# Kernel tuning notes

Measured on AMD Instinct MI355X. Metric: run time of the kernel, lower is better.

Reference implementation:

```python
import jax, jax.numpy as jnp
import numpy as np

B = 4096
D = 1024
N = 9000000
TEMPERATURE = 0.1
GAMMA = 0.8
ALPHA = 0.5
EPS = 1e-14


def setup_inputs() -> dict:
    key = jax.random.key(0)
    k1, k2, k3, k4, k5 = jax.random.split(key, 5)
    zis = jax.random.normal(k1, (B, D), dtype=jnp.float32)
    zjs = jax.random.normal(k2, (B, D), dtype=jnp.float32)
    s_I = jax.random.uniform(k3, (N,), dtype=jnp.float32)
    s_T = jax.random.uniform(k4, (N,), dtype=jnp.float32)
    b_I = jnp.zeros((N,), dtype=jnp.float32)
    b_T = jnp.zeros((N,), dtype=jnp.float32)
    ids = jax.random.randint(k5, (B,), 0, N, dtype=jnp.int64 if jax.config.jax_enable_x64 else jnp.int32)
    return {"zis": zis, "zjs": zjs, "s_I": s_I, "s_T": s_T, "b_I": b_I, "b_T": b_T, "ids": ids}


def reference(zis, zjs, s_I, s_T, b_I, b_T, ids):
    sg = jax.lax.stop_gradient
    # L2 normalize embeddings (norm=True path)
    zis = zis / jnp.linalg.norm(zis, axis=1, keepdims=True)
    zjs = zjs / jnp.linalg.norm(zjs, axis=1, keepdims=True)
    sim = jnp.einsum('id,jd->ij', zis, zjs)            # [B, B]
    diag = jnp.diagonal(sim)                            # [B]
    image_diffs = sim - diag[:, None]
    text_diffs = sim - diag[None, :]
    # detached, temperature-scaled diffs (torch .clone().detach_())
    idd = sg(image_diffs) / TEMPERATURE
    tdd = sg(text_diffs) / TEMPERATURE
    # online max tracking (per-id running max b)
    old_b_I = b_I[ids]                                  # gather [B]
    new_b_I = jnp.maximum(idd.max(axis=1), old_b_I)
    old_b_T = b_T[ids]
    new_b_T = jnp.maximum(tdd.max(axis=0), old_b_T)
    mask_neg = 1.0 - jnp.eye(B, dtype=sim.dtype)
    exp_image_diffs = jnp.exp(idd - new_b_I[:, None]) * mask_neg
    exp_text_diffs = jnp.exp(tdd - new_b_T[None, :]) * mask_neg
    g_I = exp_image_diffs.sum(axis=1) / (B - 1)         # [B]
    g_T = exp_text_diffs.sum(axis=0) / (B - 1)          # [B]
    # EMA of softmax denominator with rescaling for new max
    s_I_new = (1.0 - GAMMA) * s_I[ids] * jnp.exp(old_b_I - new_b_I) + GAMMA * g_I
    s_T_new = (1.0 - GAMMA) * s_T[ids] * jnp.exp(old_b_T - new_b_T) + GAMMA * g_T
    # state writes (side effects in torch; computed for fidelity)
    b_I = b_I.at[ids].set(new_b_I)
    b_T = b_T.at[ids].set(new_b_T)
    s_I = s_I.at[ids].set(s_I_new)
    s_T = s_T.at[ids].set(s_T_new)
    s_I_c = jnp.maximum(s_I_new, EPS)
    s_T_c = jnp.maximum(s_T_new, EPS)
    weights_image = exp_image_diffs / s_I_c[:, None]    # detached weights
    weights_text = exp_text_diffs / s_T_c[None, :]
    image_loss = (weights_image * image_diffs).sum(axis=1) / (B - 1)
    text_loss = (weights_text * text_diffs).sum(axis=0) / (B - 1)
    total_loss = ALPHA * image_loss.mean() + (1.0 - ALPHA) * text_loss.mean()
    return total_loss
```

## Files before the change

### kernel.cpp

```cpp
#include <hip/hip_runtime.h>
#include <stdint.h>

#define B_ 4096
#define D_ 1024
#define BM 256
#define BN 128
#define BK 32
#define NT 32
#define TINV 10.0f
#define LOG2E 1.4426950408889634f
#define KE (TINV * LOG2E)
#define INV_BM1 (1.0f / 4095.0f)

typedef __bf16 bf16x8 __attribute__((ext_vector_type(8)));
typedef float f32x4 __attribute__((ext_vector_type(4)));

__device__ __forceinline__ unsigned short f2bf(float x) {
  uint32_t b = __float_as_uint(x);
  b += 0x7FFF + ((b >> 16) & 1);
  return (unsigned short)(b >> 16);
}
__device__ __forceinline__ float bf2f(unsigned short u) {
  return __uint_as_float(((uint32_t)u) << 16);
}

__device__ __forceinline__ void gload16(const void* g, void* l) {
  __builtin_amdgcn_global_load_lds(
      (const __attribute__((address_space(1))) uint32_t*)g,
      (__attribute__((address_space(3))) uint32_t*)l, 16, 0, 0);
}

__global__ __launch_bounds__(256) void k_normalize(const float* __restrict__ zis,
                                                   const float* __restrict__ zjs,
                                                   unsigned short* __restrict__ Abf,
                                                   unsigned short* __restrict__ Bbf) {
  int r = blockIdx.x;
  const float* src;
  unsigned short* dst;
  if (r < B_) { src = zis + (size_t)r * D_; dst = Abf + (size_t)r * D_; }
  else        { src = zjs + (size_t)(r - B_) * D_; dst = Bbf + (size_t)(r - B_) * D_; }
  int t = threadIdx.x;
  float4 v = reinterpret_cast<const float4*>(src)[t];
  float ss = v.x*v.x + v.y*v.y + v.z*v.z + v.w*v.w;
  #pragma unroll
  for (int o = 32; o >= 1; o >>= 1) ss += __shfl_down(ss, o);
  __shared__ float red[4];
  if ((t & 63) == 0) red[t >> 6] = ss;
  __syncthreads();
  float sc = rsqrtf(red[0] + red[1] + red[2] + red[3]);
  ushort4 o4;
  o4.x = f2bf(v.x * sc); o4.y = f2bf(v.y * sc);
  o4.z = f2bf(v.z * sc); o4.w = f2bf(v.w * sc);
  reinterpret_cast<ushort4*>(dst)[t] = o4;
}

__global__ __launch_bounds__(512, 4) void k_gemm(const unsigned short* __restrict__ A,
                                                 const unsigned short* __restrict__ B,
                                                 unsigned short* __restrict__ C,
                                                 float* __restrict__ diagp) {
  __shared__ unsigned short lds[3][12288];
  const int tid = threadIdx.x;
  const int wid = tid >> 6;
  const int lane = tid & 63;
  const int wm = wid >> 1;
  const int wn = wid & 1;
  const int bRow = blockIdx.y * BM;
  const int bCol = blockIdx.x * BN;
  const unsigned short* Ag = A + (size_t)bRow * D_;
  const unsigned short* Bg = B + (size_t)bCol * D_;

  const int srowA = wid * 32 + (lane >> 2);
  const int srowB = wid * 16 + (lane >> 2);
  const int scb   = (((lane & 3) ^ ((lane >> 3) & 3))) * 8;
  const size_t soA0 = (size_t)srowA * D_ + scb;
  const size_t soA1 = (size_t)(srowA + 16) * D_ + scb;
  const size_t soB  = (size_t)srowB * D_ + scb;

  const int fr = lane & 15;
  const int kq = lane >> 4;
  const int ce = ((kq ^ ((fr >> 1) & 3)) * 8);

  f32x4 acc[4][4] = {};

#define STAGE(T, SL) {                                                        \
    const unsigned short* gA_ = Ag + (size_t)(T) * BK;                        \
    const unsigned short* gB_ = Bg + (size_t)(T) * BK;                        \
    gload16(gA_ + soA0, &lds[SL][wid * 1024]);                                \
    gload16(gA_ + soA1, &lds[SL][wid * 1024 + 512]);                          \
    gload16(gB_ + soB,  &lds[SL][8192 + wid * 512]); }

  STAGE(0, 0); STAGE(1, 1);
  asm volatile("s_waitcnt vmcnt(3)" ::: "memory");
  __builtin_amdgcn_sched_barrier(0);
  __builtin_amdgcn_s_barrier();
  __builtin_amdgcn_sched_barrier(0);

  int sl = 0, sl2 = 2;
  for (int t = 0; t < NT; ++t) {
    const unsigned short* Lb = lds[sl];
    bf16x8 a[4], b[4];
    #pragma unroll
    for (int m = 0; m < 4; ++m)
      a[m] = *reinterpret_cast<const bf16x8*>(&Lb[(wm*64 + m*16 + fr) * 32 + ce]);
    #pragma unroll
    for (int n = 0; n < 4; ++n)
      b[n] = *reinterpret_cast<const bf16x8*>(&Lb[8192 + (wn*64 + n*16 + fr) * 32 + ce]);
    if (t + 2 < NT) STAGE(t + 2, sl2);
    __builtin_amdgcn_s_setprio(1);
    #pragma unroll
    for (int m = 0; m < 4; ++m)
      #pragma unroll
      for (int n = 0; n < 4; ++n)
        acc[m][n] = __builtin_amdgcn_mfma_f32_16x16x32_bf16(a[m], b[n], acc[m][n], 0, 0, 0);
    __builtin_amdgcn_s_setprio(0);
    if (t < NT - 2) {
      asm volatile("s_waitcnt vmcnt(3)" ::: "memory");
    } else if (t == NT - 2) {
      asm volatile("s_waitcnt vmcnt(0)" ::: "memory");
    }
    __builtin_amdgcn_sched_barrier(0);
    if (t < NT - 1) {
      __builtin_amdgcn_s_barrier();
      __builtin_amdgcn_sched_barrier(0);
    }
    sl = (sl == 2) ? 0 : sl + 1;
    sl2 = (sl2 == 2) ? 0 : sl2 + 1;
  }

  const int fr4 = kq * 4;
  #pragma unroll
  for (int m = 0; m < 4; ++m)
    #pragma unroll
    for (int n = 0; n < 4; ++n)
      #pragma unroll
      for (int q = 0; q < 4; ++q) {
        float v = acc[m][n][q];
        int rg = bRow + wm * 64 + m * 16 + fr4 + q;
        int cg = bCol + wn * 64 + n * 16 + fr;
        if (rg == cg) diagp[rg] = v;
        float p = __shfl_xor(v, 1);
        if (!(lane & 1)) {
          uint32_t u = (uint32_t)f2bf(v) | ((uint32_t)f2bf(p) << 16);
          *reinterpret_cast<uint32_t*>(&C[(size_t)rg * B_ + cg]) = u;
        }
      }
#undef STAGE
}

__global__ __launch_bounds__(256) void k_fused(const unsigned short* __restrict__ sim,
    const float* __restrict__ diag,
    const float* __restrict__ bI, const float* __restrict__ sI,
    const int* __restrict__ ids,
    float* __restrict__ LI, float* __restrict__ cmax_p,
    float* __restrict__ cE_p, float* __restrict__ cE2_p) {
  const int i0 = blockIdx.x * 16;
  const int t = threadIdx.x;
  const int w = t >> 6, lane = t & 63;
  __shared__ float rowPart[16][4][3];

  float cmax[16], cE[16], cE2[16];
  #pragma unroll
  for (int k = 0; k < 16; ++k) { cmax[k] = -3.4e38f; cE[k] = 0.f; cE2[k] = 0.f; }

  for (int r = 0; r < 16; ++r) {
    const unsigned short* sp = sim + (size_t)(i0 + r) * B_ + t * 16;
    uint4 u0 = *reinterpret_cast<const uint4*>(sp);
    uint4 u1 = *reinterpret_cast<const uint4*>(sp + 8);
    float x[16];
    x[0]  = __uint_as_float(u0.x << 16); x[1]  = __uint_as_float(u0.x & 0xffff0000u);
    x[2]  = __uint_as_float(u0.y << 16); x[3]  = __uint_as_float(u0.y & 0xffff0000u);
    x[4]  = __uint_as_float(u0.z << 16); x[5]  = __uint_as_float(u0.z & 0xffff0000u);
    x[6]  = __uint_as_float(u0.w << 16); x[7]  = __uint_as_float(u0.w & 0xffff0000u);
    x[8]  = __uint_as_float(u1.x << 16); x[9]  = __uint_as_float(u1.x & 0xffff0000u);
    x[10] = __uint_as_float(u1.y << 16); x[11] = __uint_as_float(u1.y & 0xffff0000u);
    x[12] = __uint_as_float(u1.z << 16); x[13] = __uint_as_float(u1.z & 0xffff0000u);
    x[14] = __uint_as_float(u1.w << 16); x[15] = __uint_as_float(u1.w & 0xffff0000u);
    float rmx = -3.4e38f, rE = 0.f, rE2 = 0.f;
    #pragma unroll
    for (int k = 0; k < 16; ++k) {
      float e = exp2f(x[k] * KE);
      rmx = fmaxf(rmx, x[k]);
      rE += e;
      rE2 = fmaf(e, x[k], rE2);
      cmax[k] = fmaxf(cmax[k], x[k]);
      cE[k] += e;
      cE2[k] = fmaf(e, x[k], cE2[k]);
    }
    #pragma unroll
    for (int o = 32; o >= 1; o >>= 1) {
      rmx = fmaxf(rmx, __shfl_down(rmx, o));
      rE += __shfl_down(rE, o);
      rE2 += __shfl_down(rE2, o);
    }
    if (lane == 0) { rowPart[r][w][0] = rmx; rowPart[r][w][1] = rE; rowPart[r][w][2] = rE2; }
  }
  __syncthreads();
  if (t < 16) {
    int i = i0 + t;
    float mx = fmaxf(fmaxf(rowPart[t][0][0], rowPart[t][1][0]),
                     fmaxf(rowPart[t][2][0], rowPart[t][3][0]));
    float E  = (rowPart[t][0][1] + rowPart[t][1][1]) + (rowPart[t][2][1] + rowPart[t][3][1]);
    float E2 = (rowPart[t][0][2] + rowPart[t][1][2]) + (rowPart[t][2][2] + rowPart[t][3][2]);
    float dg = diag[i];
    float ed = exp2f(dg * KE);
    int id = ids[i];
    float oldb = bI[id];
    float newb = fmaxf((mx - dg) * TINV, oldb);
    float sc = exp2f(-(dg * TINV + newb) * LOG2E);
    float S1 = (E - ed) * sc;
    float S2 = (E2 - dg * E) * sc;
    float g = S1 * INV_BM1;
    float sn = 0.2f * sI[id] * exp2f((oldb - newb) * LOG2E) + 0.8f * g;
    LI[i] = S2 / fmaxf(sn, 1e-14f) * INV_BM1;
  }
  size_t base = (size_t)blockIdx.x * B_ + t * 16;
  #pragma unroll
  for (int k = 0; k < 16; ++k) {
    cmax_p[base + k] = cmax[k];
    cE_p[base + k]   = cE[k];
    cE2_p[base + k]  = cE2[k];
  }
}

__global__ __launch_bounds__(256) void k_colred(
    const float* __restrict__ diag,
    const float* __restrict__ cmax_p, const float* __restrict__ cE_p,
    const float* __restrict__ cE2_p,
    const float* __restrict__ bT, const float* __restrict__ sT,
    const int* __restrict__ ids, const float* __restrict__ LI,
    float* __restrict__ partial) {
  const int t = threadIdx.x;
  const int cidx = t >> 5;
  const int sub = t & 31;
  const int j = blockIdx.x * 8 + cidx;
  float mx = -3.4e38f, E = 0.f, E2 = 0.f;
  #pragma unroll
  for (int k = 0; k < 8; ++k) {
    size_t o = (size_t)(sub + 32 * k) * B_ + j;
    mx = fmaxf(mx, cmax_p[o]);
    E += cE_p[o];
    E2 += cE2_p[o];
  }
  #pragma unroll
  for (int o = 16; o >= 1; o >>= 1) {
    mx = fmaxf(mx, __shfl_down(mx, o, 32));
    E += __shfl_down(E, o, 32);
    E2 += __shfl_down(E2, o, 32);
  }
  __shared__ float red[8];
  if (sub == 0) {
    float dg = diag[j];
    float ed = exp2f(dg * KE);
    int id = ids[j];
    float oldb = bT[id];
    float newb = fmaxf((mx - dg) * TINV, oldb);
    float sc = exp2f(-(dg * TINV + newb) * LOG2E);
    float S1 = (E - ed) * sc;
    float S2 = (E2 - dg * E) * sc;
    float g = S1 * INV_BM1;
    float sn = 0.2f * sT[id] * exp2f((oldb - newb) * LOG2E) + 0.8f * g;
    float lt = S2 / fmaxf(sn, 1e-14f) * INV_BM1;
    red[cidx] = (0.5f * LI[j] + 0.5f * lt) * (1.0f / (float)B_);
  }
  __syncthreads();
  if (t == 0) {
    float s = 0.f;
    #pragma unroll
    for (int k = 0; k < 8; ++k) s += red[k];
    partial[blockIdx.x] = s;
  }
}

__global__ void k_final2(const float* __restrict__ partial, float* __restrict__ out) {
  int t = threadIdx.x;
  float v = partial[t];
  #pragma unroll
  for (int o = 32; o >= 1; o >>= 1) v += __shfl_down(v, o);
  __shared__ float red[8];
  if ((t & 63) == 0) red[t >> 6] = v;
  __syncthreads();
  if (t == 0) {
    float s = 0.f;
    #pragma unroll
    for (int k = 0; k < 8; ++k) s += red[k];
    out[0] = s;
  }
}

extern "C" void kernel_launch(void* const* d_in, const int* in_sizes, int n_in,
                              void* d_out, int out_size, void* d_ws, size_t ws_size,
                              hipStream_t stream) {
  const float* zis = (const float*)d_in[0];
  const float* zjs = (const float*)d_in[1];
  const float* s_I = (const float*)d_in[2];
  const float* s_T = (const float*)d_in[3];
  const float* b_I = (const float*)d_in[4];
  const float* b_T = (const float*)d_in[5];
  const int*   ids = (const int*)d_in[6];

  char* ws = (char*)d_ws;
  size_t off = 0;
  auto alloc = [&](size_t bytes) -> void* {
    void* p = ws + off;
    off = (off + bytes + 255) & ~(size_t)255;
    return p;
  };
  unsigned short* Abf = (unsigned short*)alloc((size_t)B_ * D_ * 2);
  unsigned short* Bbf = (unsigned short*)alloc((size_t)B_ * D_ * 2);
  unsigned short* sim = (unsigned short*)alloc((size_t)B_ * B_ * 2);
  float* diag   = (float*)alloc(B_ * 4);
  float* cmax_p = (float*)alloc((size_t)256 * B_ * 4);
  float* cE_p   = (float*)alloc((size_t)256 * B_ * 4);
  float* cE2_p  = (float*)alloc((size_t)256 * B_ * 4);
  float* LI     = (float*)alloc(B_ * 4);
  float* partial = (float*)alloc(512 * 4);

  k_normalize<<<2 * B_, 256, 0, stream>>>(zis, zjs, Abf, Bbf);
  k_gemm<<<dim3(B_ / BN, B_ / BM), 512, 0, stream>>>(Abf, Bbf, sim, diag);
  k_fused<<<256, 256, 0, stream>>>(sim, diag, b_I, s_I, ids, LI, cmax_p, cE_p, cE2_p);
  k_colred<<<512, 256, 0, stream>>>(diag, cmax_p, cE_p, cE2_p, b_T, s_T, ids, LI, partial);
  k_final2<<<1, 512, 0, stream>>>(partial, (float*)d_out);
}
```

Before: 91.26 us.

## Enlarge per-wave GEMM tile to 128x64 and widen fused row kernel to 1024 threads

The GEMM now runs 4 waves per 256x128 block instead of 8, so each wave computes a 128x64 output sub-tile with 32 accumulators and issues 6 global-to-LDS loads per stage. This raises MFMA work per LDS fragment read and improves register-level reuse. The cost is higher register pressure and lower occupancy. Separately, the fused row/column reduction kernel uses 1024 threads, each handling 4 columns instead of 16, which increases parallelism and memory-level concurrency but adds more partial results to combine in shared memory.

```diff
diff --git a/kernel.cpp b/kernel.cpp
--- a/kernel.cpp
+++ b/kernel.cpp
@@ -54,7 +54,7 @@
   reinterpret_cast<ushort4*>(dst)[t] = o4;
 }
 
-__global__ __launch_bounds__(512, 4) void k_gemm(const unsigned short* __restrict__ A,
+__global__ __launch_bounds__(256, 2) void k_gemm(const unsigned short* __restrict__ A,
                                                  const unsigned short* __restrict__ B,
                                                  unsigned short* __restrict__ C,
                                                  float* __restrict__ diagp) {
@@ -69,28 +69,33 @@
   const unsigned short* Ag = A + (size_t)bRow * D_;
   const unsigned short* Bg = B + (size_t)bCol * D_;
 
-  const int srowA = wid * 32 + (lane >> 2);
-  const int srowB = wid * 16 + (lane >> 2);
-  const int scb   = (((lane & 3) ^ ((lane >> 3) & 3))) * 8;
-  const size_t soA0 = (size_t)srowA * D_ + scb;
-  const size_t soA1 = (size_t)(srowA + 16) * D_ + scb;
-  const size_t soB  = (size_t)srowB * D_ + scb;
+  const int lrow = lane >> 2;
+  const int scb  = (((lane & 3) ^ ((lane >> 3) & 3))) * 8;
+  const size_t soA0 = (size_t)((wid * 4 + 0) * 16 + lrow) * D_ + scb;
+  const size_t soA1 = (size_t)((wid * 4 + 1) * 16 + lrow) * D_ + scb;
+  const size_t soA2 = (size_t)((wid * 4 + 2) * 16 + lrow) * D_ + scb;
+  const size_t soA3 = (size_t)((wid * 4 + 3) * 16 + lrow) * D_ + scb;
+  const size_t soB0 = (size_t)((wid * 2 + 0) * 16 + lrow) * D_ + scb;
+  const size_t soB1 = (size_t)((wid * 2 + 1) * 16 + lrow) * D_ + scb;
 
   const int fr = lane & 15;
   const int kq = lane >> 4;
   const int ce = ((kq ^ ((fr >> 1) & 3)) * 8);
 
-  f32x4 acc[4][4] = {};
+  f32x4 acc[8][4] = {};
 
 #define STAGE(T, SL) {                                                        \
     const unsigned short* gA_ = Ag + (size_t)(T) * BK;                        \
     const unsigned short* gB_ = Bg + (size_t)(T) * BK;                        \
-    gload16(gA_ + soA0, &lds[SL][wid * 1024]);                                \
-    gload16(gA_ + soA1, &lds[SL][wid * 1024 + 512]);                          \
-    gload16(gB_ + soB,  &lds[SL][8192 + wid * 512]); }
+    gload16(gA_ + soA0, &lds[SL][(wid * 4 + 0) * 512]);                       \
+    gload16(gA_ + soA1, &lds[SL][(wid * 4 + 1) * 512]);                       \
+    gload16(gA_ + soA2, &lds[SL][(wid * 4 + 2) * 512]);                       \
+    gload16(gA_ + soA3, &lds[SL][(wid * 4 + 3) * 512]);                       \
+    gload16(gB_ + soB0, &lds[SL][8192 + (wid * 2 + 0) * 512]);                \
+    gload16(gB_ + soB1, &lds[SL][8192 + (wid * 2 + 1) * 512]); }
 
   STAGE(0, 0); STAGE(1, 1);
-  asm volatile("s_waitcnt vmcnt(3)" ::: "memory");
+  asm volatile("s_waitcnt vmcnt(6)" ::: "memory");
   __builtin_amdgcn_sched_barrier(0);
   __builtin_amdgcn_s_barrier();
   __builtin_amdgcn_sched_barrier(0);
@@ -98,23 +103,23 @@
   int sl = 0, sl2 = 2;
   for (int t = 0; t < NT; ++t) {
     const unsigned short* Lb = lds[sl];
-    bf16x8 a[4], b[4];
-    #pragma unroll
-    for (int m = 0; m < 4; ++m)
-      a[m] = *reinterpret_cast<const bf16x8*>(&Lb[(wm*64 + m*16 + fr) * 32 + ce]);
+    bf16x8 a[8], b[4];
+    #pragma unroll
+    for (int m = 0; m < 8; ++m)
+      a[m] = *reinterpret_cast<const bf16x8*>(&Lb[(wm*128 + m*16 + fr) * 32 + ce]);
     #pragma unroll
     for (int n = 0; n < 4; ++n)
       b[n] = *reinterpret_cast<const bf16x8*>(&Lb[8192 + (wn*64 + n*16 + fr) * 32 + ce]);
     if (t + 2 < NT) STAGE(t + 2, sl2);
     __builtin_amdgcn_s_setprio(1);
     #pragma unroll
-    for (int m = 0; m < 4; ++m)
+    for (int m = 0; m < 8; ++m)
       #pragma unroll
       for (int n = 0; n < 4; ++n)
         acc[m][n] = __builtin_amdgcn_mfma_f32_16x16x32_bf16(a[m], b[n], acc[m][n], 0, 0, 0);
     __builtin_amdgcn_s_setprio(0);
     if (t < NT - 2) {
-      asm volatile("s_waitcnt vmcnt(3)" ::: "memory");
+      asm volatile("s_waitcnt vmcnt(6)" ::: "memory");
     } else if (t == NT - 2) {
       asm volatile("s_waitcnt vmcnt(0)" ::: "memory");
     }
@@ -129,13 +134,13 @@
 
   const int fr4 = kq * 4;
   #pragma unroll
-  for (int m = 0; m < 4; ++m)
+  for (int m = 0; m < 8; ++m)
     #pragma unroll
     for (int n = 0; n < 4; ++n)
       #pragma unroll
       for (int q = 0; q < 4; ++q) {
         float v = acc[m][n][q];
-        int rg = bRow + wm * 64 + m * 16 + fr4 + q;
+        int rg = bRow + wm * 128 + m * 16 + fr4 + q;
         int cg = bCol + wn * 64 + n * 16 + fr;
         if (rg == cg) diagp[rg] = v;
         float p = __shfl_xor(v, 1);
@@ -147,7 +152,7 @@
 #undef STAGE
 }
 
-__global__ __launch_bounds__(256) void k_fused(const unsigned short* __restrict__ sim,
+__global__ __launch_bounds__(1024) void k_fused(const unsigned short* __restrict__ sim,
     const float* __restrict__ diag,
     const float* __restrict__ bI, const float* __restrict__ sI,
     const int* __restrict__ ids,
@@ -156,28 +161,21 @@
   const int i0 = blockIdx.x * 16;
   const int t = threadIdx.x;
   const int w = t >> 6, lane = t & 63;
-  __shared__ float rowPart[16][4][3];
-
-  float cmax[16], cE[16], cE2[16];
-  #pragma unroll
-  for (int k = 0; k < 16; ++k) { cmax[k] = -3.4e38f; cE[k] = 0.f; cE2[k] = 0.f; }
+  __shared__ float rowPart[16][16][3];
+
+  float cmax[4], cE[4], cE2[4];
+  #pragma unroll
+  for (int k = 0; k < 4; ++k) { cmax[k] = -3.4e38f; cE[k] = 0.f; cE2[k] = 0.f; }
 
   for (int r = 0; r < 16; ++r) {
-    const unsigned short* sp = sim + (size_t)(i0 + r) * B_ + t * 16;
-    uint4 u0 = *reinterpret_cast<const uint4*>(sp);
-    uint4 u1 = *reinterpret_cast<const uint4*>(sp + 8);
-    float x[16];
-    x[0]  = __uint_as_float(u0.x << 16); x[1]  = __uint_as_float(u0.x & 0xffff0000u);
-    x[2]  = __uint_as_float(u0.y << 16); x[3]  = __uint_as_float(u0.y & 0xffff0000u);
-    x[4]  = __uint_as_float(u0.z << 16); x[5]  = __uint_as_float(u0.z & 0xffff0000u);
-    x[6]  = __uint_as_float(u0.w << 16); x[7]  = __uint_as_float(u0.w & 0xffff0000u);
-    x[8]  = __uint_as_float(u1.x << 16); x[9]  = __uint_as_float(u1.x & 0xffff0000u);
-    x[10] = __uint_as_float(u1.y << 16); x[11] = __uint_as_float(u1.y & 0xffff0000u);
-    x[12] = __uint_as_float(u1.z << 16); x[13] = __uint_as_float(u1.z & 0xffff0000u);
-    x[14] = __uint_as_float(u1.w << 16); x[15] = __uint_as_float(u1.w & 0xffff0000u);
+    const unsigned short* sp = sim + (size_t)(i0 + r) * B_ + t * 4;
+    uint2 u0 = *reinterpret_cast<const uint2*>(sp);
+    float x[4];
+    x[0] = __uint_as_float(u0.x << 16); x[1] = __uint_as_float(u0.x & 0xffff0000u);
+    x[2] = __uint_as_float(u0.y << 16); x[3] = __uint_as_float(u0.y & 0xffff0000u);
     float rmx = -3.4e38f, rE = 0.f, rE2 = 0.f;
     #pragma unroll
-    for (int k = 0; k < 16; ++k) {
+    for (int k = 0; k < 4; ++k) {
       float e = exp2f(x[k] * KE);
       rmx = fmaxf(rmx, x[k]);
       rE += e;
@@ -197,10 +195,13 @@
   __syncthreads();
   if (t < 16) {
     int i = i0 + t;
-    float mx = fmaxf(fmaxf(rowPart[t][0][0], rowPart[t][1][0]),
-                     fmaxf(rowPart[t][2][0], rowPart[t][3][0]));
-    float E  = (rowPart[t][0][1] + rowPart[t][1][1]) + (rowPart[t][2][1] + rowPart[t][3][1]);
-    float E2 = (rowPart[t][0][2] + rowPart[t][1][2]) + (rowPart[t][2][2] + rowPart[t][3][2]);
+    float mx = -3.4e38f, E = 0.f, E2 = 0.f;
+    #pragma unroll
+    for (int k = 0; k < 16; ++k) {
+      mx = fmaxf(mx, rowPart[t][k][0]);
+      E += rowPart[t][k][1];
+      E2 += rowPart[t][k][2];
+    }
     float dg = diag[i];
     float ed = exp2f(dg * KE);
     int id = ids[i];
@@ -213,9 +214,9 @@
     float sn = 0.2f * sI[id] * exp2f((oldb - newb) * LOG2E) + 0.8f * g;
     LI[i] = S2 / fmaxf(sn, 1e-14f) * INV_BM1;
   }
-  size_t base = (size_t)blockIdx.x * B_ + t * 16;
-  #pragma unroll
-  for (int k = 0; k < 16; ++k) {
+  size_t base = (size_t)blockIdx.x * B_ + t * 4;
+  #pragma unroll
+  for (int k = 0; k < 4; ++k) {
     cmax_p[base + k] = cmax[k];
     cE_p[base + k]   = cE[k];
     cE2_p[base + k]  = cE2[k];
@@ -316,8 +317,8 @@
   float* partial = (float*)alloc(512 * 4);
 
   k_normalize<<<2 * B_, 256, 0, stream>>>(zis, zjs, Abf, Bbf);
-  k_gemm<<<dim3(B_ / BN, B_ / BM), 512, 0, stream>>>(Abf, Bbf, sim, diag);
-  k_fused<<<256, 256, 0, stream>>>(sim, diag, b_I, s_I, ids, LI, cmax_p, cE_p, cE2_p);
+  k_gemm<<<dim3(B_ / BN, B_ / BM), 256, 0, stream>>>(Abf, Bbf, sim, diag);
+  k_fused<<<256, 1024, 0, stream>>>(sim, diag, b_I, s_I, ids, LI, cmax_p, cE_p, cE2_p);
   k_colred<<<512, 256, 0, stream>>>(diag, cmax_p, cE_p, cE2_p, b_T, s_T, ids, LI, partial);
   k_final2<<<1, 512, 0, stream>>>(partial, (float*)d_out);
 }
```

Measured after the change: 93.18 us. 1.02x slower.
